# Optimization experiments

Hardware: AMD Instinct MI355X
Metric: run time of the kernel (lower is better)

## Reference

```python
import jax, jax.numpy as jnp
import numpy as np

B, C, H, W = 8, 128, 64, 64


def setup_inputs() -> dict:
    key = jax.random.key(0)
    ks = jax.random.split(key, 7)
    query_img = jax.random.normal(ks[0], (B, C, H, W), dtype=jnp.float32)
    key_img = jax.random.normal(ks[1], (B, C, H, W), dtype=jnp.float32)
    value_img = jax.random.normal(ks[2], (B, C, H, W), dtype=jnp.float32)
    # 1x1 conv weights == dense [out, in] matrices (kaiming-ish scale)
    scale = 1.0 / np.sqrt(C)
    Wq = jax.random.normal(ks[3], (C, C), dtype=jnp.float32) * scale
    bq = jax.random.normal(ks[4], (C,), dtype=jnp.float32) * scale
    Wk = jax.random.normal(ks[5], (C, C), dtype=jnp.float32) * scale
    bk = jax.random.normal(ks[6], (C,), dtype=jnp.float32) * scale
    return {"query_img": query_img, "key_img": key_img, "value_img": value_img,
            "Wq": Wq, "bq": bq, "Wk": Wk, "bk": bk}


def reference(query_img, key_img, value_img, Wq, bq, Wk, bk):
    b, c, h, w = query_img.shape
    hw = h * w
    # 1x1 convs as GEMMs -> token-major layout (b, hw, c_out)
    q = jnp.einsum('bchw,oc->bhwo', query_img, Wq).reshape(b, hw, -1) + bq
    k = jnp.einsum('bchw,oc->bohw', key_img, Wk).reshape(b, -1, hw) + bk[None, :, None]
    # scores scaled by sqrt(HW) (faithful: key.size(-1) == h*w in source)
    scores = jnp.einsum('bqc,bck->bqk', q, k) / jnp.sqrt(jnp.float32(hw))
    attn = jax.nn.softmax(scores, axis=-1)  # (b, hw, hw)
    v = value_img.reshape(b, c, hw).transpose(0, 2, 1)  # (b, hw, c)
    out = jnp.einsum('bqk,bkc->bqc', attn, v)  # (b, hw, c)
    out = out.transpose(0, 2, 1).reshape(b, -1, h, w)
    out = out + q.transpose(0, 2, 1).reshape(b, -1, h, w)  # residual from query proj
    return out
```

## Files before the change

### kernel.cpp

```cpp
#include <hip/hip_runtime.h>

#define BB 8
#define CC 128
#define SS 4096
#define KT 64
#define NSPLIT 2
#define HKV (SS / NSPLIT)
#define SCALE 0.015625f

typedef __attribute__((ext_vector_type(8))) short sh8;
typedef __attribute__((ext_vector_type(4))) float f32x4;

__device__ __forceinline__ float b2f(unsigned short u) {
    union { unsigned int i; float f; } x; x.i = ((unsigned int)u) << 16; return x.f;
}
__device__ __forceinline__ unsigned short f2b(float f) {
    union { float f; unsigned int i; } x; x.f = f;
    unsigned int r = x.i + 0x7fff + ((x.i >> 16) & 1);
    return (unsigned short)(r >> 16);
}
__device__ __forceinline__ unsigned short rhu(float f) {
    union { float f; unsigned int i; } x; x.f = f;
    return (unsigned short)((x.i + 0x8000) >> 16);
}
__device__ __forceinline__ unsigned int cvtpk(float lo, float hi) {
    unsigned int r;
    asm("v_cvt_pk_bf16_f32 %0, %1, %2" : "=v"(r) : "v"(lo), "v"(hi));
    return r;
}

__device__ __forceinline__ void dma16(const void* g, void* l) {
    __builtin_amdgcn_global_load_lds((const __attribute__((address_space(1))) void*)g,
                                     (__attribute__((address_space(3))) void*)l,
                                     16, 0, 0);
}

__global__ __launch_bounds__(256) void cvt_kernel(
    const float* __restrict__ vimg,
    const float* __restrict__ Wq, const float* __restrict__ Wk,
    const float* __restrict__ bq, const float* __restrict__ bk,
    unsigned short* __restrict__ Vbuf,
    unsigned short* __restrict__ Wqb, unsigned short* __restrict__ Wkb,
    unsigned short* __restrict__ bqb, unsigned short* __restrict__ bkb)
{
    const int bx = blockIdx.x, tid = threadIdx.x;
    if (bx < 512) {
        const size_t base = (size_t)bx * 8192 + tid * 4;
        #pragma unroll
        for (int it = 0; it < 8; ++it) {
            const size_t i = base + (size_t)it * 1024;
            float4 v = *(const float4*)(vimg + i);
            ushort4 o;
            o.x = f2b(v.x); o.y = f2b(v.y); o.z = f2b(v.z); o.w = f2b(v.w);
            *(ushort4*)(Vbuf + i) = o;
        }
    } else {
        const int w = bx - 512;
        for (int e = w * 256 + tid; e < 33024; e += 2048) {
            float v; unsigned short* dst;
            if (e < 16384)      { v = Wq[e];         dst = Wqb + e; }
            else if (e < 32768) { v = Wk[e - 16384]; dst = Wkb + (e - 16384); }
            else if (e < 32896) { v = bq[e - 32768]; dst = bqb + (e - 32768); }
            else                { v = bk[e - 32896]; dst = bkb + (e - 32896); }
            *dst = f2b(v);
        }
    }
}

__global__ __launch_bounds__(256) void proj_kernel(
    const float* __restrict__ qimg, const float* __restrict__ kimg,
    const unsigned short* __restrict__ Wqb, const unsigned short* __restrict__ Wkb,
    const unsigned short* __restrict__ bqb, const unsigned short* __restrict__ bkb,
    unsigned short* __restrict__ Qbuf, unsigned short* __restrict__ Kbuf)
{
    __shared__ float ilds[128 * 69];

    const int z = blockIdx.z;
    const float* img = (z == 0) ? qimg : kimg;
    const unsigned short* Wb = (z == 0) ? Wqb : Wkb;
    const unsigned short* bias = (z == 0) ? bqb : bkb;
    unsigned short* outTok = (z == 0) ? Qbuf : Kbuf;

    const int tid  = threadIdx.x;
    const int wave = tid >> 6;
    const int lane = tid & 63;
    const int l15  = lane & 15;
    const int quad = lane >> 4;
    const int b     = blockIdx.y;
    const int stile = blockIdx.x;

    const float* gbase = img + (size_t)b * CC * SS + stile * 64;
    #pragma unroll
    for (int i = 0; i < 8; ++i) {
        const int l = tid + 256 * i;
        const int row = l >> 4, col = (l & 15) * 4;
        float4 v = *(const float4*)(gbase + (size_t)row * SS + col);
        float* d = ilds + row * 69 + col;
        d[0] = v.x; d[1] = v.y; d[2] = v.z; d[3] = v.w;
    }
    __syncthreads();

    const int tcol = wave * 16 + l15;
    sh8 a[4];
    #pragma unroll
    for (int kk = 0; kk < 4; ++kk)
        #pragma unroll
        for (int j = 0; j < 8; ++j)
            a[kk][j] = (short)rhu(ilds[(32 * kk + quad * 8 + j) * 69 + tcol]);

    f32x4 acc[8];
    #pragma unroll
    for (int nt = 0; nt < 8; ++nt) acc[nt] = (f32x4){0.f, 0.f, 0.f, 0.f};

    #pragma unroll
    for (int nt = 0; nt < 8; ++nt) {
        const unsigned short* wp = Wb + (size_t)(16 * nt + l15) * CC + quad * 8;
        #pragma unroll
        for (int kk = 0; kk < 4; ++kk) {
            sh8 bf = *(const sh8*)(wp + 32 * kk);
            acc[nt] = __builtin_amdgcn_mfma_f32_16x16x32_bf16(a[kk], bf, acc[nt], 0, 0, 0);
        }
    }

    __syncthreads();
    unsigned short* oT = (unsigned short*)ilds;
    #pragma unroll
    for (int nt = 0; nt < 8; ++nt) {
        const int o = 16 * nt + l15;
        const float bv = b2f(bias[o]);
        #pragma unroll
        for (int r = 0; r < 4; ++r) {
            const int sl = wave * 16 + quad * 4 + r;
            oT[sl * 132 + o] = f2b(acc[nt][r] + bv);
        }
    }
    __syncthreads();

    unsigned short* orow = outTok + ((size_t)b * SS + stile * 64) * CC;
    #pragma unroll
    for (int i = 0; i < 8; ++i) {
        const int idx = tid + 256 * i;
        const int s = idx >> 5, o4 = (idx & 31) * 4;
        *(ushort4*)(orow + (size_t)s * CC + o4) = *(const ushort4*)(oT + s * 132 + o4);
    }
}

__global__ __launch_bounds__(256, 2) void attn_kernel(
    const unsigned short* __restrict__ Qbuf,
    const unsigned short* __restrict__ Kbuf,
    const unsigned short* __restrict__ Vbuf,
    float* __restrict__ Oout,
    float* __restrict__ Lsum)
{
    __shared__ __align__(16) unsigned char smem[65536];

    const int tid  = threadIdx.x;
    const int wave = tid >> 6;
    const int lane = tid & 63;
    const int l15  = lane & 15;
    const int quad = lane >> 4;
    const int wgid = blockIdx.x;
    const int b    = wgid & 7;
    const int half = (wgid >> 3) & 1;
    const int qt   = wgid >> 4;
    const int qbase = qt * 128 + wave * 32;
    const int tok0  = half * HKV;

    const unsigned short* kbp = Kbuf + (size_t)b * SS * CC;
    const unsigned short* vbp = Vbuf + (size_t)b * CC * SS;

    sh8 aq[2][4];
    #pragma unroll
    for (int m = 0; m < 2; ++m) {
        const unsigned short* qp = Qbuf + ((size_t)b * SS + qbase + m * 16 + l15) * CC + quad * 8;
        #pragma unroll
        for (int kk = 0; kk < 4; ++kk) aq[m][kk] = *(const sh8*)(qp + 32 * kk);
    }

    int kGO[4], vGO[4];
    #pragma unroll
    for (int j = 0; j < 4; ++j) {
        const int krow = wave * 16 + j * 4 + quad;
        const int sx = (krow & 3) | ((krow >> 1) & 4);
        kGO[j] = krow * 256 + (((lane & 15) ^ sx) << 4);
        const int vrow = (wave * 4 + j) * 8 + (lane >> 3);
        vGO[j] = vrow * 8192 + (((lane & 7) ^ ((lane >> 3) & 7)) << 4);
    }

    int krb[4];
    #pragma unroll
    for (int n = 0; n < 4; ++n)
        krb[n] = (32 * (n >> 1) + 8 * (l15 >> 2) + 4 * (n & 1) + (l15 & 3)) * 256;
    const int krs = l15 & 7;

    f32x4 oacc[2][8];
    #pragma unroll
    for (int m = 0; m < 2; ++m)
        #pragma unroll
        for (int ct = 0; ct < 8; ++ct) oacc[m][ct] = (f32x4){0.f, 0.f, 0.f, 0.f};
    float lsum[2] = {0.f, 0.f};

    const char* gk0 = (const char*)kbp + (size_t)tok0 * 256;
    const char* gv0 = (const char*)vbp + (size_t)tok0 * 2;

    #pragma unroll
    for (int j = 0; j < 4; ++j) {
        dma16(gk0 + kGO[j], smem + (wave * 4 + j) * 1024);
        dma16(gv0 + vGO[j], smem + 32768 + (wave * 4 + j) * 1024);
    }

    for (int it = 0; it < HKV / KT; ++it) {
        unsigned char* kb = smem + ((it & 1) << 14);
        unsigned char* vb = smem + 32768 + ((it & 1) << 14);

        __syncthreads();

        if (it + 1 < HKV / KT) {
            const char* gk = gk0 + (size_t)(it + 1) * KT * 256;
            const char* gv = gv0 + (size_t)(it + 1) * KT * 2;
            unsigned char* kbn = smem + (((it + 1) & 1) << 14);
            unsigned char* vbn = smem + 32768 + (((it + 1) & 1) << 14);
            #pragma unroll
            for (int j = 0; j < 4; ++j) {
                dma16(gk + kGO[j], kbn + (wave * 4 + j) * 1024);
                dma16(gv + vGO[j], vbn + (wave * 4 + j) * 1024);
            }
        }

        f32x4 sacc[2][4];
        #pragma unroll
        for (int m = 0; m < 2; ++m)
            #pragma unroll
            for (int n = 0; n < 4; ++n) sacc[m][n] = (f32x4){0.f, 0.f, 0.f, 0.f};
        __builtin_amdgcn_s_setprio(1);
        #pragma unroll
        for (int n = 0; n < 4; ++n) {
            #pragma unroll
            for (int kk = 0; kk < 4; ++kk) {
                sh8 kf = *(const sh8*)(kb + krb[n] + (((4 * kk + quad) ^ krs) << 4));
                sacc[0][n] = __builtin_amdgcn_mfma_f32_16x16x32_bf16(kf, aq[0][kk], sacc[0][n], 0, 0, 0);
                sacc[1][n] = __builtin_amdgcn_mfma_f32_16x16x32_bf16(kf, aq[1][kk], sacc[1][n], 0, 0, 0);
            }
        }
        __builtin_amdgcn_s_setprio(0);

        union { sh8 v; unsigned int d[4]; } pa[2][2];
        #pragma unroll
        for (int m = 0; m < 2; ++m) {
            float p[4][4];
            #pragma unroll
            for (int n = 0; n < 4; ++n)
                #pragma unroll
                for (int r = 0; r < 4; ++r) {
                    p[n][r] = __expf(sacc[m][n][r] * SCALE);
                    lsum[m] += p[n][r];
                }
            #pragma unroll
            for (int kp = 0; kp < 2; ++kp) {
                pa[m][kp].d[0] = cvtpk(p[2 * kp][0],     p[2 * kp][1]);
                pa[m][kp].d[1] = cvtpk(p[2 * kp][2],     p[2 * kp][3]);
                pa[m][kp].d[2] = cvtpk(p[2 * kp + 1][0], p[2 * kp + 1][1]);
                pa[m][kp].d[3] = cvtpk(p[2 * kp + 1][2], p[2 * kp + 1][3]);
            }
        }

        __builtin_amdgcn_s_setprio(1);
        #pragma unroll
        for (int kp = 0; kp < 2; ++kp) {
            #pragma unroll
            for (int ct = 0; ct < 8; ++ct) {
                sh8 bv = *(const sh8*)(vb + (16 * ct + l15) * 128
                                          + (((kp * 4 + quad) ^ (l15 & 7)) << 4));
                oacc[0][ct] = __builtin_amdgcn_mfma_f32_16x16x32_bf16(pa[0][kp].v, bv, oacc[0][ct], 0, 0, 0);
                oacc[1][ct] = __builtin_amdgcn_mfma_f32_16x16x32_bf16(pa[1][kp].v, bv, oacc[1][ct], 0, 0, 0);
            }
        }
        __builtin_amdgcn_s_setprio(0);
    }

    #pragma unroll
    for (int m = 0; m < 2; ++m) {
        lsum[m] += __shfl_xor(lsum[m], 16, 64);
        lsum[m] += __shfl_xor(lsum[m], 32, 64);
    }
    if (quad == 0) {
        float* lp = Lsum + ((size_t)half * BB + b) * SS + qbase;
        lp[l15]      = lsum[0];
        lp[16 + l15] = lsum[1];
    }

    __syncthreads();

    unsigned short* oT = (unsigned short*)smem;
    #pragma unroll
    for (int m = 0; m < 2; ++m)
        #pragma unroll
        for (int ct = 0; ct < 8; ++ct) {
            const int c  = 16 * ct + l15;
            const int q0 = wave * 32 + m * 16 + quad * 4;
            ushort4 o;
            o.x = rhu(oacc[m][ct][0]); o.y = rhu(oacc[m][ct][1]);
            o.z = rhu(oacc[m][ct][2]); o.w = rhu(oacc[m][ct][3]);
            *(ushort4*)(oT + c * 136 + q0) = o;
        }
    __syncthreads();

    char* ob = (char*)Oout;
    #pragma unroll
    for (int i = 0; i < 16; ++i) {
        const int idx = tid + 256 * i;
        const int c = idx >> 5, q4 = (idx & 31) * 4;
        const size_t fo = ((size_t)b * CC + c) * SS + qt * 128 + q4;
        *(ushort4*)(ob + fo * 4 + 8 * half) = *(const ushort4*)(oT + c * 136 + q4);
    }
}

__global__ __launch_bounds__(256) void combine_kernel(
    const unsigned short* __restrict__ Qbuf,
    const float* __restrict__ Lsum,
    float* __restrict__ out)
{
    __shared__ unsigned short rS[64][132];
    const int b = blockIdx.y, st = blockIdx.x, tid = threadIdx.x;

    const unsigned short* qb = Qbuf + ((size_t)b * SS + st * 64) * CC;
    #pragma unroll
    for (int i = 0; i < 8; ++i) {
        const int idx = tid + 256 * i;
        const int s = idx >> 5, c4 = (idx & 31) * 4;
        *(ushort4*)(&rS[s][c4]) = *(const ushort4*)(qb + (size_t)s * CC + c4);
    }
    __syncthreads();

    const int s0l = (tid & 15) * 4;
    const int s0  = st * 64 + s0l;
    const int coff = tid >> 4;

    float4 l0 = *(const float4*)(Lsum + (size_t)b * SS + s0);
    float4 l1 = *(const float4*)(Lsum + ((size_t)BB + b) * SS + s0);
    float rinv[4];
    rinv[0] = 1.f / (l0.x + l1.x); rinv[1] = 1.f / (l0.y + l1.y);
    rinv[2] = 1.f / (l0.z + l1.z); rinv[3] = 1.f / (l0.w + l1.w);

    for (int c = coff; c < CC; c += 16) {
        const size_t po = ((size_t)b * CC + c) * SS + s0;
        uint4 u = *(const uint4*)((const char*)out + po * 4);
        float4 o;
        o.x = (b2f((unsigned short)(u.x & 0xffff)) + b2f((unsigned short)(u.z & 0xffff))) * rinv[0]
              + b2f(rS[s0l + 0][c]);
        o.y = (b2f((unsigned short)(u.x >> 16))    + b2f((unsigned short)(u.z >> 16)))    * rinv[1]
              + b2f(rS[s0l + 1][c]);
        o.z = (b2f((unsigned short)(u.y & 0xffff)) + b2f((unsigned short)(u.w & 0xffff))) * rinv[2]
              + b2f(rS[s0l + 2][c]);
        o.w = (b2f((unsigned short)(u.y >> 16))    + b2f((unsigned short)(u.w >> 16)))    * rinv[3]
              + b2f(rS[s0l + 3][c]);
        *(float4*)(out + po) = o;
    }
}

extern "C" void kernel_launch(void* const* d_in, const int* in_sizes, int n_in,
                              void* d_out, int out_size, void* d_ws, size_t ws_size,
                              hipStream_t stream) {
    const float* qimg = (const float*)d_in[0];
    const float* kimg = (const float*)d_in[1];
    const float* vimg = (const float*)d_in[2];
    const float* Wq   = (const float*)d_in[3];
    const float* bq   = (const float*)d_in[4];
    const float* Wk   = (const float*)d_in[5];
    const float* bk   = (const float*)d_in[6];
    float* out = (float*)d_out;

    unsigned short* Qbuf = (unsigned short*)d_ws;
    unsigned short* Kbuf = Qbuf + (size_t)BB * SS * CC;
    unsigned short* Vbuf = Kbuf + (size_t)BB * SS * CC;
    unsigned short* Wqb  = Vbuf + (size_t)BB * SS * CC;
    unsigned short* Wkb  = Wqb + CC * CC;
    unsigned short* bqb  = Wkb + CC * CC;
    unsigned short* bkb  = bqb + CC;
    float* Lsum = (float*)(bkb + CC);

    cvt_kernel<<<dim3(520), 256, 0, stream>>>(vimg, Wq, Wk, bq, bk,
                                              Vbuf, Wqb, Wkb, bqb, bkb);
    proj_kernel<<<dim3(SS / 64, BB, 2), 256, 0, stream>>>(
        qimg, kimg, Wqb, Wkb, bqb, bkb, Qbuf, Kbuf);
    attn_kernel<<<dim3(NSPLIT * BB * (SS / 128)), 256, 0, stream>>>(
        Qbuf, Kbuf, Vbuf, out, Lsum);
    combine_kernel<<<dim3(SS / 64, BB), 256, 0, stream>>>(Qbuf, Lsum, out);
}
```

Measured before the change: 194.6 us.

## Software-pipeline QK of next tile against softmax and PV of current tile

Restructures the attention main loop so the QK MFMAs for tile it+1 are issued after the softmax and PV of tile it, using two alternating score accumulator sets. K tiles are now prefetched two iterations ahead in a double buffer, while V drops to a single buffer reloaded between PV and the next QK. This cuts LDS use from 64KB to 48KB per block and aims to overlap exp/convert work with matrix-core work. In exchange it keeps more live registers and hides V load latency only behind one QK phase.

```diff
diff --git a/kernel.cpp b/kernel.cpp
--- a/kernel.cpp
+++ b/kernel.cpp
@@ -6,6 +6,7 @@
 #define KT 64
 #define NSPLIT 2
 #define HKV (SS / NSPLIT)
+#define NIT (HKV / KT)
 #define SCALE 0.015625f
 
 typedef __attribute__((ext_vector_type(8))) short sh8;
@@ -152,7 +153,7 @@
     float* __restrict__ Oout,
     float* __restrict__ Lsum)
 {
-    __shared__ __align__(16) unsigned char smem[65536];
+    __shared__ __align__(16) unsigned char smem[49152];
 
     const int tid  = threadIdx.x;
     const int wave = tid >> 6;
@@ -203,48 +204,28 @@
     const char* gk0 = (const char*)kbp + (size_t)tok0 * 256;
     const char* gv0 = (const char*)vbp + (size_t)tok0 * 2;
 
-    #pragma unroll
-    for (int j = 0; j < 4; ++j) {
-        dma16(gk0 + kGO[j], smem + (wave * 4 + j) * 1024);
-        dma16(gv0 + vGO[j], smem + 32768 + (wave * 4 + j) * 1024);
-    }
-
-    for (int it = 0; it < HKV / KT; ++it) {
+    typedef union { sh8 v; unsigned int d[4]; } paU;
+    f32x4 saccA[2][4], saccB[2][4];
+
+    auto QK = [&](int it, f32x4 (&dst)[2][4]) {
         unsigned char* kb = smem + ((it & 1) << 14);
-        unsigned char* vb = smem + 32768 + ((it & 1) << 14);
-
-        __syncthreads();
-
-        if (it + 1 < HKV / KT) {
-            const char* gk = gk0 + (size_t)(it + 1) * KT * 256;
-            const char* gv = gv0 + (size_t)(it + 1) * KT * 2;
-            unsigned char* kbn = smem + (((it + 1) & 1) << 14);
-            unsigned char* vbn = smem + 32768 + (((it + 1) & 1) << 14);
-            #pragma unroll
-            for (int j = 0; j < 4; ++j) {
-                dma16(gk + kGO[j], kbn + (wave * 4 + j) * 1024);
-                dma16(gv + vGO[j], vbn + (wave * 4 + j) * 1024);
-            }
-        }
-
-        f32x4 sacc[2][4];
         #pragma unroll
         for (int m = 0; m < 2; ++m)
             #pragma unroll
-            for (int n = 0; n < 4; ++n) sacc[m][n] = (f32x4){0.f, 0.f, 0.f, 0.f};
+            for (int n = 0; n < 4; ++n) dst[m][n] = (f32x4){0.f, 0.f, 0.f, 0.f};
         __builtin_amdgcn_s_setprio(1);
         #pragma unroll
         for (int n = 0; n < 4; ++n) {
             #pragma unroll
             for (int kk = 0; kk < 4; ++kk) {
                 sh8 kf = *(const sh8*)(kb + krb[n] + (((4 * kk + quad) ^ krs) << 4));
-                sacc[0][n] = __builtin_amdgcn_mfma_f32_16x16x32_bf16(kf, aq[0][kk], sacc[0][n], 0, 0, 0);
-                sacc[1][n] = __builtin_amdgcn_mfma_f32_16x16x32_bf16(kf, aq[1][kk], sacc[1][n], 0, 0, 0);
+                dst[0][n] = __builtin_amdgcn_mfma_f32_16x16x32_bf16(kf, aq[0][kk], dst[0][n], 0, 0, 0);
+                dst[1][n] = __builtin_amdgcn_mfma_f32_16x16x32_bf16(kf, aq[1][kk], dst[1][n], 0, 0, 0);
             }
         }
         __builtin_amdgcn_s_setprio(0);
-
-        union { sh8 v; unsigned int d[4]; } pa[2][2];
+    };
+    auto SM = [&](f32x4 (&src)[2][4], paU (&pa)[2][2]) {
         #pragma unroll
         for (int m = 0; m < 2; ++m) {
             float p[4][4];
@@ -252,7 +233,7 @@
             for (int n = 0; n < 4; ++n)
                 #pragma unroll
                 for (int r = 0; r < 4; ++r) {
-                    p[n][r] = __expf(sacc[m][n][r] * SCALE);
+                    p[n][r] = __expf(src[m][n][r] * SCALE);
                     lsum[m] += p[n][r];
                 }
             #pragma unroll
@@ -263,7 +244,9 @@
                 pa[m][kp].d[3] = cvtpk(p[2 * kp + 1][2], p[2 * kp + 1][3]);
             }
         }
-
+    };
+    auto PV = [&](paU (&pa)[2][2]) {
+        unsigned char* vb = smem + 32768;
         __builtin_amdgcn_s_setprio(1);
         #pragma unroll
         for (int kp = 0; kp < 2; ++kp) {
@@ -276,6 +259,48 @@
             }
         }
         __builtin_amdgcn_s_setprio(0);
+    };
+
+    #pragma unroll
+    for (int j = 0; j < 4; ++j) {
+        dma16(gk0 + kGO[j], smem + (wave * 4 + j) * 1024);
+        dma16(gv0 + vGO[j], smem + 32768 + (wave * 4 + j) * 1024);
+    }
+    __syncthreads();
+    {
+        const char* gk = gk0 + (size_t)KT * 256;
+        #pragma unroll
+        for (int j = 0; j < 4; ++j)
+            dma16(gk + kGO[j], smem + 16384 + (wave * 4 + j) * 1024);
+    }
+    QK(0, saccA);
+
+    for (int it = 0; it < NIT - 1; ++it) {
+        __syncthreads();
+        if (it <= NIT - 3) {
+            const char* gk = gk0 + (size_t)(it + 2) * KT * 256;
+            unsigned char* kbn = smem + ((it & 1) << 14);
+            #pragma unroll
+            for (int j = 0; j < 4; ++j)
+                dma16(gk + kGO[j], kbn + (wave * 4 + j) * 1024);
+        }
+        paU pa[2][2];
+        if (it & 1) SM(saccB, pa); else SM(saccA, pa);
+        PV(pa);
+        __syncthreads();
+        {
+            const char* gv = gv0 + (size_t)(it + 1) * KT * 2;
+            #pragma unroll
+            for (int j = 0; j < 4; ++j)
+                dma16(gv + vGO[j], smem + 32768 + (wave * 4 + j) * 1024);
+        }
+        if (it & 1) QK(it + 1, saccA); else QK(it + 1, saccB);
+    }
+    __syncthreads();
+    {
+        paU pa[2][2];
+        SM(saccB, pa);
+        PV(pa);
     }
 
     #pragma unroll
```

Result: no change. 197.1 us (+1.3%).
